# Kernel tuning notes

Measured on AMD Instinct MI355X. Metric: run time of the kernel, lower is better.

The kernel has to match this reference:

```python
import jax, jax.numpy as jnp
import numpy as np

N_NODES = 100000
N_EDGES = 1000000
C_IN = 64
C_OUT = 64


def setup_inputs() -> dict:
    key = jax.random.key(0)
    k1, k2, k3 = jax.random.split(key, 3)
    x = jax.random.normal(k1, (N_NODES, C_IN), dtype=jnp.float32)
    edge_index = jax.random.randint(k2, (2, N_EDGES), 0, N_NODES, dtype=jnp.int64)
    # glorot-scaled weight, zero bias (as in GCNConv defaults)
    scale = jnp.sqrt(2.0 / (C_IN + C_OUT)).astype(jnp.float32)
    W = jax.random.normal(k3, (C_IN, C_OUT), dtype=jnp.float32) * scale
    b = jnp.zeros((C_OUT,), dtype=jnp.float32)
    return {"x": x, "edge_index": edge_index, "W": W, "b": b}


def reference(x, edge_index, W, b):
    # GCNConv: out = D^{-1/2} (A + I) D^{-1/2} (x W) + b
    n = x.shape[0]
    # add self loops
    loop = jnp.arange(n, dtype=edge_index.dtype)
    src = jnp.concatenate([edge_index[0], loop])  # [E+N]
    dst = jnp.concatenate([edge_index[1], loop])  # [E+N]
    # degree of A_hat computed over destination (col) nodes, edge_weight = 1
    ones = jnp.ones(src.shape[0], dtype=x.dtype)
    deg = jax.ops.segment_sum(ones, dst, num_segments=n)  # [N]
    deg_inv_sqrt = jnp.where(deg > 0, jax.lax.rsqrt(deg), 0.0)
    norm = deg_inv_sqrt[src] * deg_inv_sqrt[dst]  # [E+N]
    # linear transform, then gather-scale-scatter aggregation
    h = x @ W  # [N, C_OUT]
    msg = norm[:, None] * h[src]  # [E+N, C_OUT]
    out = jax.ops.segment_sum(msg, dst, num_segments=n)  # [N, C_OUT]
    return out + b
```

## Files before the change

kernel.cpp:

```cpp
#include <hip/hip_runtime.h>
#include <hip/hip_bf16.h>

#define C 64

__device__ __forceinline__ float bflo(unsigned u) { return __uint_as_float(u << 16); }
__device__ __forceinline__ float bfhi(unsigned u) { return __uint_as_float(u & 0xffff0000u); }
__device__ __forceinline__ unsigned bfrne(float f) {
    unsigned u = __float_as_uint(f);
    return (u + 0x7fffu + ((u >> 16) & 1u)) >> 16;
}

__global__ void zero_kernel(uint4* __restrict__ p, int n4) {
    int i = blockIdx.x * blockDim.x + threadIdx.x;
    if (i < n4) p[i] = make_uint4(0u, 0u, 0u, 0u);
}

__global__ void count_deg_kernel(const int* __restrict__ dst, unsigned* __restrict__ deg,
                                 unsigned* __restrict__ rank, int E) {
    int e = blockIdx.x * blockDim.x + threadIdx.x;
    if (e < E) {
        rank[e] = atomicAdd(&deg[dst[e]], 1u);
    }
}

__global__ void scan1_kernel(const unsigned* __restrict__ deg, unsigned* __restrict__ offs,
                             unsigned* __restrict__ bsum, float* __restrict__ dis, int n) {
    __shared__ unsigned s[256];
    int t = threadIdx.x;
    int base = blockIdx.x * 1024 + t * 4;
    unsigned v0 = 0, v1 = 0, v2 = 0, v3 = 0;
    if (base + 0 < n) v0 = deg[base + 0];
    if (base + 1 < n) v1 = deg[base + 1];
    if (base + 2 < n) v2 = deg[base + 2];
    if (base + 3 < n) v3 = deg[base + 3];
    if (base + 0 < n) dis[base + 0] = rsqrtf((float)(v0 + 1u));
    if (base + 1 < n) dis[base + 1] = rsqrtf((float)(v1 + 1u));
    if (base + 2 < n) dis[base + 2] = rsqrtf((float)(v2 + 1u));
    if (base + 3 < n) dis[base + 3] = rsqrtf((float)(v3 + 1u));
    s[t] = v0 + v1 + v2 + v3;
    __syncthreads();
    for (int d = 1; d < 256; d <<= 1) {
        unsigned val = (t >= d) ? s[t - d] : 0u;
        __syncthreads();
        s[t] += val;
        __syncthreads();
    }
    unsigned excl = (t == 0) ? 0u : s[t - 1];
    if (t == 255) bsum[blockIdx.x] = s[255];
    if (base + 0 < n) offs[base + 0] = excl;
    if (base + 1 < n) offs[base + 1] = excl + v0;
    if (base + 2 < n) offs[base + 2] = excl + v0 + v1;
    if (base + 3 < n) offs[base + 3] = excl + v0 + v1 + v2;
}

__global__ void scan2_kernel(unsigned* __restrict__ bsum, int nb) {
    __shared__ unsigned s[256];
    int t = threadIdx.x;
    s[t] = (t < nb) ? bsum[t] : 0u;
    __syncthreads();
    for (int d = 1; d < 256; d <<= 1) {
        unsigned val = (t >= d) ? s[t - d] : 0u;
        __syncthreads();
        s[t] += val;
        __syncthreads();
    }
    if (t < nb) bsum[t] = (t == 0) ? 0u : s[t - 1];
}

__global__ void bucket_kernel(const int* __restrict__ src, const int* __restrict__ dst,
                              const unsigned* __restrict__ offs, const unsigned* __restrict__ bsum,
                              const unsigned* __restrict__ rank, unsigned* __restrict__ ssrc, int E) {
    int e = blockIdx.x * blockDim.x + threadIdx.x;
    if (e < E) {
        int d = dst[e];
        unsigned pos = offs[d] + bsum[d >> 10] + rank[e];
        ssrc[pos] = (unsigned)src[e];
    }
}

__global__ void __launch_bounds__(256, 4)
gemm64_kernel(const float* __restrict__ x, const float* __restrict__ W,
              const float* __restrict__ dis, unsigned short* __restrict__ hsb, int n) {
    __shared__ float Xl[64][68];
    __shared__ float Wl[64][64];
    int tid = threadIdx.x;
    int rbase = blockIdx.x * 64;
    for (int i = tid; i < 1024; i += 256) {
        ((float4*)Wl)[i] = ((const float4*)W)[i];
    }
    for (int i = tid; i < 1024; i += 256) {
        int r = i >> 4, kq = i & 15;
        float4 v;
        if (rbase + r < n) v = ((const float4*)(x + (size_t)(rbase + r) * C))[kq];
        else               v = make_float4(0.f, 0.f, 0.f, 0.f);
        *(float4*)&Xl[r][kq * 4] = v;
    }
    __syncthreads();

    int tx = tid & 15;
    int ty = tid >> 4;
    float4 acc[4];
    #pragma unroll
    for (int j = 0; j < 4; ++j) acc[j] = make_float4(0.f, 0.f, 0.f, 0.f);

    #pragma unroll 2
    for (int kb = 0; kb < 16; ++kb) {
        float4 wv0 = *(const float4*)&Wl[kb * 4 + 0][tx * 4];
        float4 wv1 = *(const float4*)&Wl[kb * 4 + 1][tx * 4];
        float4 wv2 = *(const float4*)&Wl[kb * 4 + 2][tx * 4];
        float4 wv3 = *(const float4*)&Wl[kb * 4 + 3][tx * 4];
        #pragma unroll
        for (int j = 0; j < 4; ++j) {
            float4 xv = *(const float4*)&Xl[ty * 4 + j][kb * 4];
            acc[j].x = fmaf(xv.x, wv0.x, acc[j].x);
            acc[j].y = fmaf(xv.x, wv0.y, acc[j].y);
            acc[j].z = fmaf(xv.x, wv0.z, acc[j].z);
            acc[j].w = fmaf(xv.x, wv0.w, acc[j].w);
            acc[j].x = fmaf(xv.y, wv1.x, acc[j].x);
            acc[j].y = fmaf(xv.y, wv1.y, acc[j].y);
            acc[j].z = fmaf(xv.y, wv1.z, acc[j].z);
            acc[j].w = fmaf(xv.y, wv1.w, acc[j].w);
            acc[j].x = fmaf(xv.z, wv2.x, acc[j].x);
            acc[j].y = fmaf(xv.z, wv2.y, acc[j].y);
            acc[j].z = fmaf(xv.z, wv2.z, acc[j].z);
            acc[j].w = fmaf(xv.z, wv2.w, acc[j].w);
            acc[j].x = fmaf(xv.w, wv3.x, acc[j].x);
            acc[j].y = fmaf(xv.w, wv3.y, acc[j].y);
            acc[j].z = fmaf(xv.w, wv3.z, acc[j].z);
            acc[j].w = fmaf(xv.w, wv3.w, acc[j].w);
        }
    }
    #pragma unroll
    for (int j = 0; j < 4; ++j) {
        int row = rbase + ty * 4 + j;
        if (row < n) {
            float d = dis[row];
            unsigned p0 = bfrne(acc[j].x * d) | (bfrne(acc[j].y * d) << 16);
            unsigned p1 = bfrne(acc[j].z * d) | (bfrne(acc[j].w * d) << 16);
            ((uint2*)(hsb + (size_t)row * C))[tx] = make_uint2(p0, p1);
        }
    }
}

__global__ void gather_kernel(const unsigned* __restrict__ offs, const unsigned* __restrict__ bsum,
                              const unsigned* __restrict__ deg, const unsigned* __restrict__ ssrc,
                              const float* __restrict__ dis, const unsigned short* __restrict__ hsb,
                              const float* __restrict__ b, float* __restrict__ out, int n) {
    int node = blockIdx.x * 4 + (threadIdx.x >> 6);
    if (node >= n) return;
    int lane = threadIdx.x & 63;
    int g = lane >> 3;
    int l = lane & 7;
    unsigned off = offs[node] + bsum[node >> 10];
    unsigned dg  = deg[node];
    float a0 = 0.f, a1 = 0.f, a2 = 0.f, a3 = 0.f, a4 = 0.f, a5 = 0.f, a6 = 0.f, a7 = 0.f;
    unsigned k = 0;
    for (; k + 16 <= dg; k += 16) {
        unsigned s0 = ssrc[off + k + g];
        unsigned s1 = ssrc[off + k + 8 + g];
        uint4 v0 = ((const uint4*)(hsb + (size_t)s0 * C))[l];
        uint4 v1 = ((const uint4*)(hsb + (size_t)s1 * C))[l];
        a0 += bflo(v0.x) + bflo(v1.x); a1 += bfhi(v0.x) + bfhi(v1.x);
        a2 += bflo(v0.y) + bflo(v1.y); a3 += bfhi(v0.y) + bfhi(v1.y);
        a4 += bflo(v0.z) + bflo(v1.z); a5 += bfhi(v0.z) + bfhi(v1.z);
        a6 += bflo(v0.w) + bflo(v1.w); a7 += bfhi(v0.w) + bfhi(v1.w);
    }
    if (k + 8 <= dg) {
        unsigned s0 = ssrc[off + k + g];
        uint4 v0 = ((const uint4*)(hsb + (size_t)s0 * C))[l];
        a0 += bflo(v0.x); a1 += bfhi(v0.x);
        a2 += bflo(v0.y); a3 += bfhi(v0.y);
        a4 += bflo(v0.z); a5 += bfhi(v0.z);
        a6 += bflo(v0.w); a7 += bfhi(v0.w);
        k += 8;
    }
    if (k + g < dg) {
        unsigned s0 = ssrc[off + k + g];
        uint4 v0 = ((const uint4*)(hsb + (size_t)s0 * C))[l];
        a0 += bflo(v0.x); a1 += bfhi(v0.x);
        a2 += bflo(v0.y); a3 += bfhi(v0.y);
        a4 += bflo(v0.z); a5 += bfhi(v0.z);
        a6 += bflo(v0.w); a7 += bfhi(v0.w);
    }
    #pragma unroll
    for (int m = 8; m <= 32; m <<= 1) {
        a0 += __shfl_xor(a0, m); a1 += __shfl_xor(a1, m);
        a2 += __shfl_xor(a2, m); a3 += __shfl_xor(a3, m);
        a4 += __shfl_xor(a4, m); a5 += __shfl_xor(a5, m);
        a6 += __shfl_xor(a6, m); a7 += __shfl_xor(a7, m);
    }
    if (g < 2) {
        float di = dis[node];
        uint4 u = ((const uint4*)(hsb + (size_t)node * C))[l];
        unsigned w0 = (g == 0) ? u.x : u.z;
        unsigned w1 = (g == 0) ? u.y : u.w;
        float s0 = bflo(w0), s1 = bfhi(w0), s2 = bflo(w1), s3 = bfhi(w1);
        float e0 = (g == 0) ? a0 : a4;
        float e1 = (g == 0) ? a1 : a5;
        float e2 = (g == 0) ? a2 : a6;
        float e3 = (g == 0) ? a3 : a7;
        float4 bv = ((const float4*)b)[l * 2 + g];
        float4 o;
        o.x = di * (s0 + e0) + bv.x;
        o.y = di * (s1 + e1) + bv.y;
        o.z = di * (s2 + e2) + bv.z;
        o.w = di * (s3 + e3) + bv.w;
        ((float4*)(out + (size_t)node * C))[l * 2 + g] = o;
    }
}

extern "C" void kernel_launch(void* const* d_in, const int* in_sizes, int n_in,
                              void* d_out, int out_size, void* d_ws, size_t ws_size,
                              hipStream_t stream) {
    const float* x   = (const float*)d_in[0];
    const int*   ei  = (const int*)d_in[1];
    const float* W   = (const float*)d_in[2];
    const float* b   = (const float*)d_in[3];
    float*       out = (float*)d_out;

    const int N = in_sizes[0] / C;
    const int E = in_sizes[1] / 2;
    const int* src = ei;
    const int* dst = ei + E;

    char* ws = (char*)d_ws;
    size_t o = 0;
    auto carve = [&](size_t bytes) { char* p = ws + o; o = (o + bytes + 255) & ~(size_t)255; return p; };
    unsigned* deg       = (unsigned*)carve((size_t)N * 4);
    unsigned* offs      = (unsigned*)carve((size_t)N * 4);
    unsigned* bsum      = (unsigned*)carve(1024 * 4);
    float*    dis       = (float*)carve((size_t)N * 4);
    unsigned* rank      = (unsigned*)carve((size_t)E * 4);
    unsigned* ssrc      = (unsigned*)carve((size_t)E * 4);
    unsigned short* hsb = (unsigned short*)carve((size_t)N * C * 2);

    int n4 = (N + 3) / 4;
    zero_kernel<<<(n4 + 255) / 256, 256, 0, stream>>>((uint4*)deg, n4);

    count_deg_kernel<<<(E + 255) / 256, 256, 0, stream>>>(dst, deg, rank, E);

    int nb = (N + 1023) / 1024;
    scan1_kernel<<<nb, 256, 0, stream>>>(deg, offs, bsum, dis, N);
    scan2_kernel<<<1, 256, 0, stream>>>(bsum, nb);

    bucket_kernel<<<(E + 255) / 256, 256, 0, stream>>>(src, dst, offs, bsum, rank, ssrc, E);

    gemm64_kernel<<<(N + 63) / 64, 256, 0, stream>>>(x, W, dis, hsb, N);

    gather_kernel<<<(N + 3) / 4, 256, 0, stream>>>(offs, bsum, deg, ssrc, dis, hsb, b, out, N);
}
```

Before: 130.1 us.

## Partition degree counters per XCC to keep atomics local to each die

Replaces the single global degree array with eight per-XCC partitioned counter arrays, selected by reading the hardware XCC id, and does the atomic adds at workgroup scope so they stay in the local L2 instead of contending across dies. The scan kernel folds the partitions into per-node degrees and writes per-partition exclusive prefixes back in place, and the bucket kernel adds the partition prefix to each edge's rank. This trades a larger zeroed workspace and extra reads in scan and bucket for cheaper atomics. Correctness relies on workgroup-scope atomics being coherent among all blocks on the same XCC, and on the rank bit packing leaving 27 bits for per-partition counts.

New measurement: 131.2 us. Within noise of the previous version (+0.9%).

```diff
diff --git a/kernel.cpp b/kernel.cpp
--- a/kernel.cpp
+++ b/kernel.cpp
@@ -10,33 +10,67 @@
     return (u + 0x7fffu + ((u >> 16) & 1u)) >> 16;
 }
 
+__device__ __forceinline__ unsigned xcc_id() {
+    return __builtin_amdgcn_s_getreg(6164) & 7u;
+}
+
 __global__ void zero_kernel(uint4* __restrict__ p, int n4) {
     int i = blockIdx.x * blockDim.x + threadIdx.x;
     if (i < n4) p[i] = make_uint4(0u, 0u, 0u, 0u);
 }
 
-__global__ void count_deg_kernel(const int* __restrict__ dst, unsigned* __restrict__ deg,
-                                 unsigned* __restrict__ rank, int E) {
+__global__ void count_part_kernel(const int* __restrict__ dst, unsigned* __restrict__ part,
+                                  int S, unsigned* __restrict__ rank, int E) {
     int e = blockIdx.x * blockDim.x + threadIdx.x;
     if (e < E) {
-        rank[e] = atomicAdd(&deg[dst[e]], 1u);
-    }
-}
-
-__global__ void scan1_kernel(const unsigned* __restrict__ deg, unsigned* __restrict__ offs,
+        unsigned x = xcc_id();
+        unsigned d = (unsigned)dst[e];
+        unsigned r = __hip_atomic_fetch_add(&part[x * (unsigned)S + d], 1u,
+                                            __ATOMIC_RELAXED, __HIP_MEMORY_SCOPE_WORKGROUP);
+        rank[e] = (x << 27) | r;
+    }
+}
+
+__global__ void scan1_kernel(unsigned* __restrict__ part, int S,
+                             unsigned* __restrict__ deg, unsigned* __restrict__ offs,
                              unsigned* __restrict__ bsum, float* __restrict__ dis, int n) {
     __shared__ unsigned s[256];
     int t = threadIdx.x;
     int base = blockIdx.x * 1024 + t * 4;
     unsigned v0 = 0, v1 = 0, v2 = 0, v3 = 0;
-    if (base + 0 < n) v0 = deg[base + 0];
-    if (base + 1 < n) v1 = deg[base + 1];
-    if (base + 2 < n) v2 = deg[base + 2];
-    if (base + 3 < n) v3 = deg[base + 3];
-    if (base + 0 < n) dis[base + 0] = rsqrtf((float)(v0 + 1u));
-    if (base + 1 < n) dis[base + 1] = rsqrtf((float)(v1 + 1u));
-    if (base + 2 < n) dis[base + 2] = rsqrtf((float)(v2 + 1u));
-    if (base + 3 < n) dis[base + 3] = rsqrtf((float)(v3 + 1u));
+    if (base + 4 <= n) {
+        uint4 run = make_uint4(0u, 0u, 0u, 0u);
+        #pragma unroll
+        for (int x = 0; x < 8; ++x) {
+            uint4* p = (uint4*)&part[(size_t)x * S + base];
+            uint4 v = *p;
+            *p = run;
+            run.x += v.x; run.y += v.y; run.z += v.z; run.w += v.w;
+        }
+        v0 = run.x; v1 = run.y; v2 = run.z; v3 = run.w;
+        *(uint4*)&deg[base] = run;
+        dis[base + 0] = rsqrtf((float)(v0 + 1u));
+        dis[base + 1] = rsqrtf((float)(v1 + 1u));
+        dis[base + 2] = rsqrtf((float)(v2 + 1u));
+        dis[base + 3] = rsqrtf((float)(v3 + 1u));
+    } else if (base < n) {
+        for (int j = 0; j < 4; ++j) {
+            int i = base + j;
+            if (i >= n) break;
+            unsigned run = 0;
+            #pragma unroll
+            for (int x = 0; x < 8; ++x) {
+                unsigned* p = &part[(size_t)x * S + i];
+                unsigned v = *p;
+                *p = run;
+                run += v;
+            }
+            deg[i] = run;
+            dis[i] = rsqrtf((float)(run + 1u));
+            if (j == 0) v0 = run; else if (j == 1) v1 = run;
+            else if (j == 2) v2 = run; else v3 = run;
+        }
+    }
     s[t] = v0 + v1 + v2 + v3;
     __syncthreads();
     for (int d = 1; d < 256; d <<= 1) {
@@ -69,11 +103,14 @@
 
 __global__ void bucket_kernel(const int* __restrict__ src, const int* __restrict__ dst,
                               const unsigned* __restrict__ offs, const unsigned* __restrict__ bsum,
+                              const unsigned* __restrict__ part, int S,
                               const unsigned* __restrict__ rank, unsigned* __restrict__ ssrc, int E) {
     int e = blockIdx.x * blockDim.x + threadIdx.x;
     if (e < E) {
-        int d = dst[e];
-        unsigned pos = offs[d] + bsum[d >> 10] + rank[e];
+        unsigned d = (unsigned)dst[e];
+        unsigned u = rank[e];
+        unsigned x = u >> 27;
+        unsigned pos = offs[d] + bsum[d >> 10] + part[(size_t)x * S + d] + (u & 0x07FFFFFFu);
         ssrc[pos] = (unsigned)src[e];
     }
 }
@@ -223,9 +260,12 @@
     const int* src = ei;
     const int* dst = ei + E;
 
+    const int S = (N + 63) & ~63;
+
     char* ws = (char*)d_ws;
     size_t o = 0;
     auto carve = [&](size_t bytes) { char* p = ws + o; o = (o + bytes + 255) & ~(size_t)255; return p; };
+    unsigned* part      = (unsigned*)carve((size_t)8 * S * 4);
     unsigned* deg       = (unsigned*)carve((size_t)N * 4);
     unsigned* offs      = (unsigned*)carve((size_t)N * 4);
     unsigned* bsum      = (unsigned*)carve(1024 * 4);
@@ -234,16 +274,16 @@
     unsigned* ssrc      = (unsigned*)carve((size_t)E * 4);
     unsigned short* hsb = (unsigned short*)carve((size_t)N * C * 2);
 
-    int n4 = (N + 3) / 4;
-    zero_kernel<<<(n4 + 255) / 256, 256, 0, stream>>>((uint4*)deg, n4);
-
-    count_deg_kernel<<<(E + 255) / 256, 256, 0, stream>>>(dst, deg, rank, E);
+    int n4 = 2 * S;
+    zero_kernel<<<(n4 + 255) / 256, 256, 0, stream>>>((uint4*)part, n4);
+
+    count_part_kernel<<<(E + 255) / 256, 256, 0, stream>>>(dst, part, S, rank, E);
 
     int nb = (N + 1023) / 1024;
-    scan1_kernel<<<nb, 256, 0, stream>>>(deg, offs, bsum, dis, N);
+    scan1_kernel<<<nb, 256, 0, stream>>>(part, S, deg, offs, bsum, dis, N);
     scan2_kernel<<<1, 256, 0, stream>>>(bsum, nb);
 
-    bucket_kernel<<<(E + 255) / 256, 256, 0, stream>>>(src, dst, offs, bsum, rank, ssrc, E);
+    bucket_kernel<<<(E + 255) / 256, 256, 0, stream>>>(src, dst, offs, bsum, part, S, rank, ssrc, E);
 
     gemm64_kernel<<<(N + 63) / 64, 256, 0, stream>>>(x, W, dis, hsb, N);
 
```
